# Kernel optimization log

Hardware: AMD Instinct MI355X
Metric: run time of the kernel (lower is better)

Reference implementation:

```python
import jax, jax.numpy as jnp
import numpy as np

N_HEAD = 12

def setup_inputs() -> dict:
    key = jax.random.key(0)
    k1, k2, k3 = jax.random.split(key, 3)
    B, T, E = 4, 2048, 768
    x = jax.random.normal(k1, (B, T, E), dtype=jnp.float32)
    Wqkv = jax.random.normal(k2, (E, 3 * E), dtype=jnp.float32) * 0.02
    Wproj = jax.random.normal(k3, (E, E), dtype=jnp.float32) * 0.02
    return {"x": x, "Wqkv": Wqkv, "Wproj": Wproj}

def reference(x, Wqkv, Wproj):
    B, T, E = x.shape
    H = N_HEAD
    hd = E // H
    qkv = x @ Wqkv                                  # [B,T,3E]
    q, k, v = jnp.split(qkv, 3, axis=-1)
    # [B,T,E] -> [B,H,T,hd]
    q = q.reshape(B, T, H, hd).transpose(0, 2, 1, 3)
    k = k.reshape(B, T, H, hd).transpose(0, 2, 1, 3)
    v = v.reshape(B, T, H, hd).transpose(0, 2, 1, 3)
    scores = jnp.einsum("bhqd,bhkd->bhqk", q, k) / jnp.sqrt(jnp.float32(hd))
    # original: masked_fill(tril(scores)==0, -inf) == causal mask (upper triangle zeroed by tril)
    masked = jnp.where(jnp.tril(scores) == 0, -jnp.inf, scores)
    attn = jax.nn.softmax(masked, axis=-1)
    out = jnp.einsum("bhqk,bhkd->bhqd", attn, v)    # [B,H,T,hd]
    out = out.transpose(0, 2, 1, 3).reshape(B, T, E)
    return out @ Wproj
```

## Files before the change

kernel.cpp:

```cpp
#include <hip/hip_runtime.h>
#include <hip/hip_bf16.h>


#define BB 4
#define TT 2048
#define EE 768
#define HH 12
#define HD 64
#define KK 768
#define BTE (BB*TT*EE)

typedef __attribute__((ext_vector_type(8))) short bf16x8;
typedef __attribute__((ext_vector_type(4))) float f32x4;
typedef __attribute__((ext_vector_type(16))) float f32x16;
typedef __attribute__((ext_vector_type(4))) int i32x4;

#define QSC 0.18033688011112042f
#define THR2 11.5f

#define GLOAD16(gp, lp) \
    __builtin_amdgcn_global_load_lds( \
        (const __attribute__((address_space(1))) unsigned*)(gp), \
        (__attribute__((address_space(3))) unsigned*)(lp), 16, 0, 0)

static __device__ __forceinline__ unsigned short f2bf(float f) {
    unsigned u = __builtin_bit_cast(unsigned, f);
    u += 0x7fffu + ((u >> 16) & 1u);
    return (unsigned short)(u >> 16);
}

static __device__ __forceinline__ unsigned cvt_pk_bf16(float lo, float hi) {
    unsigned r;
    asm("v_cvt_pk_bf16_f32 %0, %1, %2" : "=v"(r) : "v"(lo), "v"(hi));
    return r;
}

__global__ __launch_bounds__(256)
void convx_kernel(const float* __restrict__ x, unsigned short* __restrict__ xb) {
    const size_t i = ((size_t)blockIdx.x * 256 + threadIdx.x) * 8;
    float4 a = *(const float4*)&x[i];
    float4 b = *(const float4*)&x[i + 4];
    ushort4 lo, hi;
    lo.x = f2bf(a.x); lo.y = f2bf(a.y); lo.z = f2bf(a.z); lo.w = f2bf(a.w);
    hi.x = f2bf(b.x); hi.y = f2bf(b.y); hi.z = f2bf(b.z); hi.w = f2bf(b.w);
    *(ushort4*)&xb[i] = lo;
    *(ushort4*)&xb[i + 4] = hi;
}

__global__ __launch_bounds__(256)
void transw_kernel(const float* __restrict__ W, unsigned short* __restrict__ Wt, int N) {
    __shared__ unsigned short Ts[64][72];
    const int n0 = blockIdx.x * 64;
    const int k0 = blockIdx.y * 64;
    const int tid = threadIdx.x;
    {
        const int r = tid >> 4;
        const int c4 = (tid & 15) << 2;
#pragma unroll
        for (int i = 0; i < 4; ++i) {
            const int k = r + i * 16;
            float4 w4 = *(const float4*)&W[(size_t)(k0 + k) * N + n0 + c4];
            Ts[k][c4 + 0] = f2bf(w4.x); Ts[k][c4 + 1] = f2bf(w4.y);
            Ts[k][c4 + 2] = f2bf(w4.z); Ts[k][c4 + 3] = f2bf(w4.w);
        }
    }
    __syncthreads();
#pragma unroll
    for (int i = 0; i < 2; ++i) {
        const int idx = tid + i * 256;
        const int n = idx >> 3;
        const int ch = idx & 7;
        ushort4 p0, p1;
        p0.x = Ts[ch * 8 + 0][n]; p0.y = Ts[ch * 8 + 1][n];
        p0.z = Ts[ch * 8 + 2][n]; p0.w = Ts[ch * 8 + 3][n];
        p1.x = Ts[ch * 8 + 4][n]; p1.y = Ts[ch * 8 + 5][n];
        p1.z = Ts[ch * 8 + 6][n]; p1.w = Ts[ch * 8 + 7][n];
        *(ushort4*)&Wt[(size_t)(n0 + n) * KK + k0 + ch * 8] = p0;
        *(ushort4*)&Wt[(size_t)(n0 + n) * KK + k0 + ch * 8 + 4] = p1;
    }
}

template<int MODE>
__global__ __launch_bounds__(256)
void mfma_gemm_kernel(const unsigned short* __restrict__ A,
                      const unsigned short* __restrict__ Wt,
                      unsigned short* __restrict__ q_ws,
                      unsigned short* __restrict__ k_ws,
                      unsigned short* __restrict__ v_ws,
                      float* __restrict__ outf) {
    __shared__ __align__(16) unsigned short As[128 * 32];
    __shared__ __align__(16) unsigned short Bs[128 * 32];
    const int bx = blockIdx.x;
    const int by = blockIdx.y;
    const int tid = threadIdx.x;
    const int w = tid >> 6, lane = tid & 63;
    const int c = lane & 15, g = lane >> 4;
    const int wr = w >> 1, wc = w & 1;
    const int m0 = by * 128, n0 = bx * 128;

    const int lrow = lane >> 2;
    const int lch  = (lane & 3) * 8;

    const unsigned short* Ap = A  + (size_t)m0 * KK;
    const unsigned short* Bp = Wt + (size_t)n0 * KK;

    f32x4 acc[4][4] = {};

    for (int kt = 0; kt < KK / 32; ++kt) {
        const int k0 = kt * 32;
        __syncthreads();
        GLOAD16(Ap + (size_t)(w * 32 +  0 + lrow) * KK + k0 + lch, &As[(w * 32 +  0) * 32]);
        GLOAD16(Ap + (size_t)(w * 32 + 16 + lrow) * KK + k0 + lch, &As[(w * 32 + 16) * 32]);
        GLOAD16(Bp + (size_t)(w * 32 +  0 + lrow) * KK + k0 + lch, &Bs[(w * 32 +  0) * 32]);
        GLOAD16(Bp + (size_t)(w * 32 + 16 + lrow) * KK + k0 + lch, &Bs[(w * 32 + 16) * 32]);
        __syncthreads();

        bf16x8 af[4], bfr[4];
#pragma unroll
        for (int m = 0; m < 4; ++m)
            af[m] = *(const bf16x8*)&As[(wr * 64 + m * 16 + c) * 32 + g * 8];
#pragma unroll
        for (int n = 0; n < 4; ++n)
            bfr[n] = *(const bf16x8*)&Bs[(wc * 64 + n * 16 + c) * 32 + g * 8];
#pragma unroll
        for (int m = 0; m < 4; ++m)
#pragma unroll
            for (int n = 0; n < 4; ++n)
                acc[m][n] = __builtin_amdgcn_mfma_f32_16x16x32_bf16(af[m], bfr[n], acc[m][n], 0, 0, 0);
    }

    if (MODE == 0) {
        const int which = n0 / EE;
        const int hh = (n0 % EE) / HD + wc;
        const int bb = m0 / TT;
        const int tb = (m0 % TT) + wr * 64;
        const int bh = bb * HH + hh;
        if (which < 2) {
            const float sc_ = (which == 0) ? QSC : 1.0f;
            unsigned short* dst = (which == 0) ? q_ws : k_ws;
#pragma unroll
            for (int m = 0; m < 4; ++m) {
                const int t32 = (tb >> 5) + (m >> 1);
#pragma unroll
                for (int n = 0; n < 4; ++n) {
                    unsigned short* base = dst
                        + ((size_t)(bh * (TT / 32) + t32) * 4 + n) * 512
                        + ((m & 1) * 16 + 4 * g + 32 * (c >> 3)) * 8 + (c & 7);
#pragma unroll
                    for (int j = 0; j < 4; ++j)
                        base[j * 8] = f2bf(acc[m][n][j] * sc_);
                }
            }
        } else {
            unsigned short* vb = v_ws + ((size_t)(bh * (TT / 64) + (tb >> 6))) * 4096;
#pragma unroll
            for (int m = 0; m < 4; ++m)
#pragma unroll
                for (int n = 0; n < 4; ++n) {
                    unsigned short* base = vb + ((size_t)(n >> 1) * 4 + m) * 512
                        + ((n & 1) * 16 + c + 32 * (g >> 1)) * 8 + 4 * (g & 1);
                    ushort4 pk;
                    pk.x = f2bf(acc[m][n][0]); pk.y = f2bf(acc[m][n][1]);
                    pk.z = f2bf(acc[m][n][2]); pk.w = f2bf(acc[m][n][3]);
                    *(ushort4*)base = pk;
                }
        }
    } else {
#pragma unroll
        for (int m = 0; m < 4; ++m)
#pragma unroll
            for (int n = 0; n < 4; ++n)
#pragma unroll
                for (int j = 0; j < 4; ++j)
                    outf[(size_t)(m0 + wr * 64 + m * 16 + 4 * g + j) * EE
                         + n0 + wc * 64 + n * 16 + c] = acc[m][n][j];
    }
}

__global__ __launch_bounds__(64)
void attn_kernel(const unsigned short* __restrict__ qf,
                 const unsigned short* __restrict__ kfr,
                 const unsigned short* __restrict__ vfr,
                 unsigned short* __restrict__ attn_b) {
    const int bh = blockIdx.x;
    const int j = (TT / 32 - 1) - (int)blockIdx.y;
    const int b = bh / HH, h = bh % HH;
    const int lane = threadIdx.x;
    const int lq = lane & 31;
    const int hiL = lane >> 5;

    const int q0 = j * 32;
    const int qg = q0 + lq;

    const unsigned short* qbase = qf + ((size_t)(bh * (TT / 32) + j)) * 2048;
    bf16x8 qa[4];
#pragma unroll
    for (int ds = 0; ds < 4; ++ds)
        qa[ds] = *(const bf16x8*)&qbase[ds * 512 + lane * 8];

    const unsigned short* kfb = kfr + (size_t)bh * 131072;
    const unsigned short* vfb = vfr + (size_t)bh * 131072;

    const i32x4 onesw = {0x3F803F80, 0x3F803F80, 0x3F803F80, 0x3F803F80};
    const bf16x8 ones = __builtin_bit_cast(bf16x8, onesw);

    f32x16 o0 = {}, o1 = {}, ol = {};
    float m_r = -INFINITY;

    const int ktiles = (j >> 1) + 1;

    for (int kt = 0; kt < ktiles; ++kt) {
        const int kv0 = kt * 64;

        bf16x8 kf[8], vf[8];
        {
            const unsigned short* kc = kfb + ((size_t)(2 * kt) * 4) * 512 + lane * 8;
#pragma unroll
            for (int ch = 0; ch < 8; ++ch)
                kf[ch] = *(const bf16x8*)&kc[ch * 512];
            const unsigned short* vc = vfb + (size_t)kt * 4096 + lane * 8;
#pragma unroll
            for (int ch = 0; ch < 8; ++ch)
                vf[ch] = *(const bf16x8*)&vc[ch * 512];
        }

        f32x16 s0 = {}, s1 = {};
        __builtin_amdgcn_s_setprio(1);
#pragma unroll
        for (int ds = 0; ds < 4; ++ds) {
            s0 = __builtin_amdgcn_mfma_f32_32x32x16_bf16(kf[ds],     qa[ds], s0, 0, 0, 0);
            s1 = __builtin_amdgcn_mfma_f32_32x32x16_bf16(kf[4 + ds], qa[ds], s1, 0, 0, 0);
        }
        __builtin_amdgcn_s_setprio(0);

        if (kv0 + 63 > q0) {
#pragma unroll
            for (int r = 0; r < 16; ++r) {
                const int crow = (r & 3) + 8 * (r >> 2) + 4 * hiL;
                if (kv0 + crow > qg)      s0[r] = -INFINITY;
                if (kv0 + 32 + crow > qg) s1[r] = -INFINITY;
            }
        }

        float t[16];
#pragma unroll
        for (int r = 0; r < 16; ++r) t[r] = fmaxf(s0[r], s1[r]);
        const float a0 = fmaxf(fmaxf(t[0], t[1]), t[2]);
        const float a1 = fmaxf(fmaxf(t[3], t[4]), t[5]);
        const float a2 = fmaxf(fmaxf(t[6], t[7]), t[8]);
        const float a3 = fmaxf(fmaxf(t[9], t[10]), t[11]);
        const float a4 = fmaxf(fmaxf(t[12], t[13]), t[14]);
        float mx = fmaxf(fmaxf(fmaxf(a0, a1), a2), fmaxf(fmaxf(a3, a4), t[15]));
        mx = fmaxf(mx, __shfl_xor(mx, 32));

        if (!__all(mx <= m_r + THR2)) {
            const float mn = fmaxf(m_r, mx);
            const float alpha = __builtin_amdgcn_exp2f(m_r - mn);
            m_r = mn;
#pragma unroll
            for (int r = 0; r < 16; ++r) {
                const float al = __shfl(alpha, (r & 3) + 8 * (r >> 2) + 4 * hiL);
                o0[r] *= al; o1[r] *= al; ol[r] *= al;
            }
        }

#pragma unroll
        for (int r = 0; r < 16; ++r) s0[r] = __builtin_amdgcn_exp2f(s0[r] - m_r);
#pragma unroll
        for (int r = 0; r < 16; ++r) s1[r] = __builtin_amdgcn_exp2f(s1[r] - m_r);

        __builtin_amdgcn_s_setprio(1);
#define PACKSTEP(E0,E1,E2,E3,E4,E5,E6,E7, VK) do { \
        const unsigned wlo0 = cvt_pk_bf16(E0, E1); \
        const unsigned wlo1 = cvt_pk_bf16(E2, E3); \
        const unsigned whi0 = cvt_pk_bf16(E4, E5); \
        const unsigned whi1 = cvt_pk_bf16(E6, E7); \
        const unsigned g0 = (unsigned)__shfl_xor((int)(hiL ? wlo0 : whi0), 32); \
        const unsigned g1 = (unsigned)__shfl_xor((int)(hiL ? wlo1 : whi1), 32); \
        i32x4 pw; \
        pw[0] = (int)(hiL ? g0 : wlo0); \
        pw[1] = (int)(hiL ? g1 : wlo1); \
        pw[2] = (int)(hiL ? whi0 : g0); \
        pw[3] = (int)(hiL ? whi1 : g1); \
        const bf16x8 pa = __builtin_bit_cast(bf16x8, pw); \
        o0 = __builtin_amdgcn_mfma_f32_32x32x16_bf16(pa, vf[VK],     o0, 0, 0, 0); \
        o1 = __builtin_amdgcn_mfma_f32_32x32x16_bf16(pa, vf[4 + VK], o1, 0, 0, 0); \
        ol = __builtin_amdgcn_mfma_f32_32x32x16_bf16(pa, ones,       ol, 0, 0, 0); \
    } while (0)

        PACKSTEP(s0[0], s0[1], s0[2], s0[3], s0[4], s0[5], s0[6], s0[7], 0);
        PACKSTEP(s0[8], s0[9], s0[10], s0[11], s0[12], s0[13], s0[14], s0[15], 1);
        PACKSTEP(s1[0], s1[1], s1[2], s1[3], s1[4], s1[5], s1[6], s1[7], 2);
        PACKSTEP(s1[8], s1[9], s1[10], s1[11], s1[12], s1[13], s1[14], s1[15], 3);
#undef PACKSTEP
        __builtin_amdgcn_s_setprio(0);
    }

    unsigned short* op = attn_b + ((size_t)b * TT + q0) * EE + h * HD;
#pragma unroll
    for (int r = 0; r < 16; ++r) {
        const int crow = (r & 3) + 8 * (r >> 2) + 4 * hiL;
        const float li = 1.f / ol[r];
        op[(size_t)crow * EE + lq]      = f2bf(o0[r] * li);
        op[(size_t)crow * EE + 32 + lq] = f2bf(o1[r] * li);
    }
}

extern "C" void kernel_launch(void* const* d_in, const int* in_sizes, int n_in,
                              void* d_out, int out_size, void* d_ws, size_t ws_size,
                              hipStream_t stream) {
    const float* x     = (const float*)d_in[0];
    const float* wqkv  = (const float*)d_in[1];
    const float* wproj = (const float*)d_in[2];
    float* out = (float*)d_out;

    unsigned short* ws = (unsigned short*)d_ws;
    unsigned short* q_ws    = ws;
    unsigned short* k_ws    = ws + (size_t)BTE;
    unsigned short* v_ws    = ws + 2 * (size_t)BTE;
    unsigned short* xb      = ws + 3 * (size_t)BTE;
    unsigned short* attn_b  = ws + 4 * (size_t)BTE;
    unsigned short* wqkv_t  = ws + 5 * (size_t)BTE;
    unsigned short* wproj_t = wqkv_t + (size_t)2304 * 768;

    convx_kernel<<<BTE / 2048, 256, 0, stream>>>(x, xb);
    transw_kernel<<<dim3(2304 / 64, KK / 64), 256, 0, stream>>>(wqkv, wqkv_t, 2304);
    transw_kernel<<<dim3(768 / 64, KK / 64), 256, 0, stream>>>(wproj, wproj_t, 768);

    mfma_gemm_kernel<0><<<dim3(2304 / 128, 8192 / 128), 256, 0, stream>>>(
        xb, wqkv_t, q_ws, k_ws, v_ws, nullptr);
    attn_kernel<<<dim3(BB * HH, TT / 32), 64, 0, stream>>>(q_ws, k_ws, v_ws, attn_b);
    mfma_gemm_kernel<1><<<dim3(EE / 128, 8192 / 128), 256, 0, stream>>>(
        attn_b, wproj_t, nullptr, nullptr, nullptr, out);
}
```

Before: 143.4 us.

## Double-buffer GEMM LDS tiles and swizzle workgroup order across XCDs

Both GEMMs (QKV projection and output projection) now use two LDS buffers. The global-to-LDS load for the next K tile is issued before the MFMA work on the current tile, and only one barrier is used per iteration. This is meant to hide global load latency behind compute. The block index is also remapped so that consecutive workgroups, which are dispatched round-robin across the 8 XCDs, share tiles within an XCD for better L2 reuse. LDS use doubles, and the swizzle assumes the grid size is divisible by 8.

```diff
diff --git a/kernel.cpp b/kernel.cpp
--- a/kernel.cpp
+++ b/kernel.cpp
@@ -88,10 +88,16 @@
                       unsigned short* __restrict__ k_ws,
                       unsigned short* __restrict__ v_ws,
                       float* __restrict__ outf) {
-    __shared__ __align__(16) unsigned short As[128 * 32];
-    __shared__ __align__(16) unsigned short Bs[128 * 32];
-    const int bx = blockIdx.x;
-    const int by = blockIdx.y;
+    __shared__ __align__(16) unsigned short As[2][128 * 32];
+    __shared__ __align__(16) unsigned short Bs[2][128 * 32];
+
+    const int nwg = gridDim.x * gridDim.y;
+    const int orig = blockIdx.y * gridDim.x + blockIdx.x;
+    const int cpx = nwg >> 3;
+    const int swz = (orig & 7) * cpx + (orig >> 3);
+    const int bx = swz % gridDim.x;
+    const int by = swz / gridDim.x;
+
     const int tid = threadIdx.x;
     const int w = tid >> 6, lane = tid & 63;
     const int c = lane & 15, g = lane >> 4;
@@ -105,29 +111,39 @@
     const unsigned short* Bp = Wt + (size_t)n0 * KK;
 
     f32x4 acc[4][4] = {};
-
-    for (int kt = 0; kt < KK / 32; ++kt) {
-        const int k0 = kt * 32;
-        __syncthreads();
-        GLOAD16(Ap + (size_t)(w * 32 +  0 + lrow) * KK + k0 + lch, &As[(w * 32 +  0) * 32]);
-        GLOAD16(Ap + (size_t)(w * 32 + 16 + lrow) * KK + k0 + lch, &As[(w * 32 + 16) * 32]);
-        GLOAD16(Bp + (size_t)(w * 32 +  0 + lrow) * KK + k0 + lch, &Bs[(w * 32 +  0) * 32]);
-        GLOAD16(Bp + (size_t)(w * 32 + 16 + lrow) * KK + k0 + lch, &Bs[(w * 32 + 16) * 32]);
-        __syncthreads();
+    const int NT = KK / 32;
+
+#define GSTAGE(pp, kt_) do { const int k0_ = (kt_) * 32; \
+        GLOAD16(Ap + (size_t)(w * 32 +  0 + lrow) * KK + k0_ + lch, &As[pp][(w * 32 +  0) * 32]); \
+        GLOAD16(Ap + (size_t)(w * 32 + 16 + lrow) * KK + k0_ + lch, &As[pp][(w * 32 + 16) * 32]); \
+        GLOAD16(Bp + (size_t)(w * 32 +  0 + lrow) * KK + k0_ + lch, &Bs[pp][(w * 32 +  0) * 32]); \
+        GLOAD16(Bp + (size_t)(w * 32 + 16 + lrow) * KK + k0_ + lch, &Bs[pp][(w * 32 + 16) * 32]); \
+    } while (0)
+
+    GSTAGE(0, 0);
+    __syncthreads();
+    int p = 0;
+
+    for (int kt = 0; kt < NT; ++kt) {
+        if (kt + 1 < NT) GSTAGE(p ^ 1, kt + 1);
 
         bf16x8 af[4], bfr[4];
 #pragma unroll
         for (int m = 0; m < 4; ++m)
-            af[m] = *(const bf16x8*)&As[(wr * 64 + m * 16 + c) * 32 + g * 8];
+            af[m] = *(const bf16x8*)&As[p][(wr * 64 + m * 16 + c) * 32 + g * 8];
 #pragma unroll
         for (int n = 0; n < 4; ++n)
-            bfr[n] = *(const bf16x8*)&Bs[(wc * 64 + n * 16 + c) * 32 + g * 8];
+            bfr[n] = *(const bf16x8*)&Bs[p][(wc * 64 + n * 16 + c) * 32 + g * 8];
 #pragma unroll
         for (int m = 0; m < 4; ++m)
 #pragma unroll
             for (int n = 0; n < 4; ++n)
                 acc[m][n] = __builtin_amdgcn_mfma_f32_16x16x32_bf16(af[m], bfr[n], acc[m][n], 0, 0, 0);
-    }
+
+        __syncthreads();
+        p ^= 1;
+    }
+#undef GSTAGE
 
     if (MODE == 0) {
         const int which = n0 / EE;
```

Measured after the change: 138.8 us. 1.03x faster.
